# Performance work log

Measured on AMD Instinct MI355X. Metric: run time of the kernel, lower is better.

## Reference

```python
import jax, jax.numpy as jnp
import numpy as np


def setup_inputs() -> dict:
    key = jax.random.key(0)
    x = jax.random.normal(key, (16, 1, 1536, 1536), dtype=jnp.float32)
    return {"x": x, "kernel_size": 3}


def reference(x, kernel_size):
    # MaxPool2d(k, stride=k, return_indices) + MaxUnpool2d: keep only the
    # per-block argmax value in each non-overlapping k x k block, zero elsewhere.
    B, C, H, W = x.shape
    k = kernel_size
    Hk, Wk = H // k, W // k
    # [B,C,Hk,Wk,k*k] view of non-overlapping blocks
    xb = x.reshape(B, C, Hk, k, Wk, k).transpose(0, 1, 2, 4, 3, 5).reshape(B, C, Hk, Wk, k * k)
    idx = jnp.argmax(xb, axis=-1)  # first max per block, matches torch pool indices
    keep = idx[..., None] == jnp.arange(k * k)  # one-hot mask [B,C,Hk,Wk,k*k]
    out = jnp.where(keep, xb, jnp.zeros((), dtype=x.dtype))
    # scatter back to the original layout
    out = out.reshape(B, C, Hk, Wk, k, k).transpose(0, 1, 2, 4, 3, 5).reshape(B, C, H, W)
    return out
```

## Files before the change

kernel.cpp:

```cpp
#include <hip/hip_runtime.h>


#define IMG_H 1536
#define IMG_W 1536
#define N_IMG 16
#define HK    512
#define WK4   128

__global__ __launch_bounds__(256) void pool_nms_kernel(const float* __restrict__ x,
                                                       float* __restrict__ out) {
    const int tid = blockIdx.x * 256 + threadIdx.x;
    const int bw4 = tid & (WK4 - 1);
    const int t2  = tid >> 7;
    const int bh  = t2 & (HK - 1);
    const int n   = t2 >> 9;

    const size_t base = (size_t)n * (IMG_H * (size_t)IMG_W)
                      + (size_t)(bh * 3) * IMG_W
                      + (size_t)bw4 * 12;

    float row[3][12];
#pragma unroll
    for (int r = 0; r < 3; ++r) {
        const float* p = x + base + (size_t)r * IMG_W;
#pragma unroll
        for (int j = 0; j < 3; ++j) {
            float4 t = *(const float4*)(p + j * 4);
            row[r][j * 4 + 0] = t.x;
            row[r][j * 4 + 1] = t.y;
            row[r][j * 4 + 2] = t.z;
            row[r][j * 4 + 3] = t.w;
        }
    }

    float o[3][12];
#pragma unroll
    for (int s = 0; s < 4; ++s) {
        const int c0 = s * 3;
        float best = row[0][c0];
        int bi = 0;
#pragma unroll
        for (int r = 0; r < 3; ++r) {
#pragma unroll
            for (int c = 0; c < 3; ++c) {
                const float vv = row[r][c0 + c];
                if (vv > best) { best = vv; bi = r * 3 + c; }
            }
        }
#pragma unroll
        for (int r = 0; r < 3; ++r) {
#pragma unroll
            for (int c = 0; c < 3; ++c) {
                o[r][c0 + c] = ((r * 3 + c) == bi) ? row[r][c0 + c] : 0.0f;
            }
        }
    }

#pragma unroll
    for (int r = 0; r < 3; ++r) {
        float* p = out + base + (size_t)r * IMG_W;
#pragma unroll
        for (int j = 0; j < 3; ++j) {
            *(float4*)(p + j * 4) = make_float4(o[r][j * 4 + 0], o[r][j * 4 + 1],
                                                o[r][j * 4 + 2], o[r][j * 4 + 3]);
        }
    }
}

extern "C" void kernel_launch(void* const* d_in, const int* in_sizes, int n_in,
                              void* d_out, int out_size, void* d_ws, size_t ws_size,
                              hipStream_t stream) {
    const float* x = (const float*)d_in[0];
    float* out = (float*)d_out;
    const int n_threads = N_IMG * HK * WK4;
    pool_nms_kernel<<<n_threads / 256, 256, 0, stream>>>(x, out);
}
```

Before: 262.7 us.

## Stage 6-row tiles through LDS for fully coalesced global loads and stores

Each workgroup now copies a 6-row tile of the image into shared memory with contiguous float4 loads, runs the 3x3 block argmax out of LDS, writes the masked results back to LDS, then stores the tile to global memory with contiguous float4 writes. The old per-thread 48-byte strided float4 accesses were only partly coalesced, and this staging replaces them with fully coalesced streaming. The cost is 36 KB of LDS per workgroup, which limits occupancy, two barriers, and LDS bank conflicts from the 12-float stride of the per-thread access.

Result: faster. 257.5 us (-2.0%).

```diff
diff --git a/kernel.cpp b/kernel.cpp
--- a/kernel.cpp
+++ b/kernel.cpp
@@ -4,32 +4,44 @@
 #define IMG_H 1536
 #define IMG_W 1536
 #define N_IMG 16
-#define HK    512
-#define WK4   128
+#define TILE_ROWS 6
+#define TILE_F (TILE_ROWS * IMG_W)
+#define TILE_V (TILE_F / 4)
+#define V_PER_T (TILE_V / 256)
+#define TILES_PER_IMG (IMG_H / TILE_ROWS)
 
 __global__ __launch_bounds__(256) void pool_nms_kernel(const float* __restrict__ x,
                                                        float* __restrict__ out) {
-    const int tid = blockIdx.x * 256 + threadIdx.x;
-    const int bw4 = tid & (WK4 - 1);
-    const int t2  = tid >> 7;
-    const int bh  = t2 & (HK - 1);
-    const int n   = t2 >> 9;
+    __shared__ float lds[TILE_F];
 
+    const int wg = blockIdx.x;
+    const int n  = wg >> 8;
+    const int tr = wg & (TILES_PER_IMG - 1);
     const size_t base = (size_t)n * (IMG_H * (size_t)IMG_W)
-                      + (size_t)(bh * 3) * IMG_W
-                      + (size_t)bw4 * 12;
+                      + (size_t)(tr * TILE_ROWS) * IMG_W;
+    const int t = threadIdx.x;
 
+    const float4* xin = (const float4*)(x + base);
+#pragma unroll
+    for (int k = 0; k < V_PER_T; ++k) {
+        const int v = t + k * 256;
+        ((float4*)lds)[v] = xin[v];
+    }
+    __syncthreads();
+
+    const int br = t >> 7;
+    const int g  = t & 127;
     float row[3][12];
 #pragma unroll
     for (int r = 0; r < 3; ++r) {
-        const float* p = x + base + (size_t)r * IMG_W;
+        const float* p = lds + (br * 3 + r) * IMG_W + g * 12;
 #pragma unroll
         for (int j = 0; j < 3; ++j) {
-            float4 t = *(const float4*)(p + j * 4);
-            row[r][j * 4 + 0] = t.x;
-            row[r][j * 4 + 1] = t.y;
-            row[r][j * 4 + 2] = t.z;
-            row[r][j * 4 + 3] = t.w;
+            float4 v4 = *(const float4*)(p + j * 4);
+            row[r][j * 4 + 0] = v4.x;
+            row[r][j * 4 + 1] = v4.y;
+            row[r][j * 4 + 2] = v4.z;
+            row[r][j * 4 + 3] = v4.w;
         }
     }
 
@@ -58,12 +70,20 @@
 
 #pragma unroll
     for (int r = 0; r < 3; ++r) {
-        float* p = out + base + (size_t)r * IMG_W;
+        float* p = lds + (br * 3 + r) * IMG_W + g * 12;
 #pragma unroll
         for (int j = 0; j < 3; ++j) {
             *(float4*)(p + j * 4) = make_float4(o[r][j * 4 + 0], o[r][j * 4 + 1],
                                                 o[r][j * 4 + 2], o[r][j * 4 + 3]);
         }
+    }
+    __syncthreads();
+
+    float4* po = (float4*)(out + base);
+#pragma unroll
+    for (int k = 0; k < V_PER_T; ++k) {
+        const int v = t + k * 256;
+        po[v] = ((const float4*)lds)[v];
     }
 }
 
@@ -72,6 +92,6 @@
                               hipStream_t stream) {
     const float* x = (const float*)d_in[0];
     float* out = (float*)d_out;
-    const int n_threads = N_IMG * HK * WK4;
-    pool_nms_kernel<<<n_threads / 256, 256, 0, stream>>>(x, out);
+    const int n_wg = N_IMG * TILES_PER_IMG;
+    pool_nms_kernel<<<n_wg, 256, 0, stream>>>(x, out);
 }
```

## Remap threads to contiguous float4 columns with wave shuffles for block halos

Applied to the files above, without the earlier changes.

Each wavefront now covers a 256-column span of one 3-row band, and each lane loads one contiguous float4 per row, so global loads and stores are fully coalesced instead of strided 48-byte chunks per thread. Neighbouring columns of each 3x3 block are gathered with shuffle-up and shuffle-down, plus extra edge loads at span boundaries. Each lane redundantly recomputes the first-max test for every block it touches using prefix and suffix maxima. This trades extra ALU work, shuffles and halo loads for better memory coalescing.

New measurement: 258.7 us. About the same (-1.5%).

```diff
diff --git a/kernel.cpp b/kernel.cpp
--- a/kernel.cpp
+++ b/kernel.cpp
@@ -1,69 +1,100 @@
 #include <hip/hip_runtime.h>
+#include <math.h>
 
 
 #define IMG_H 1536
 #define IMG_W 1536
 #define N_IMG 16
-#define HK    512
-#define WK4   128
+#define SPANS 6
+#define BROWS 512
+
+typedef float __attribute__((ext_vector_type(4))) f32x4;
 
 __global__ __launch_bounds__(256) void pool_nms_kernel(const float* __restrict__ x,
                                                        float* __restrict__ out) {
-    const int tid = blockIdx.x * 256 + threadIdx.x;
-    const int bw4 = tid & (WK4 - 1);
-    const int t2  = tid >> 7;
-    const int bh  = t2 & (HK - 1);
-    const int n   = t2 >> 9;
+    const int lane = threadIdx.x & 63;
+    const int wid  = blockIdx.x * 4 + (threadIdx.x >> 6);
+    const int W  = wid % SPANS;
+    const int t2 = wid / SPANS;
+    const int R  = t2 & (BROWS - 1);
+    const int n  = t2 >> 9;
 
     const size_t base = (size_t)n * (IMG_H * (size_t)IMG_W)
-                      + (size_t)(bh * 3) * IMG_W
-                      + (size_t)bw4 * 12;
+                      + (size_t)(R * 3) * IMG_W;
+    const int c0 = W * 256;
+    const float* px = x + base + c0;
 
-    float row[3][12];
+    f32x4 own[3];
+#pragma unroll
+    for (int r = 0; r < 3; ++r)
+        own[r] = *(const f32x4*)(px + (size_t)r * IMG_W + lane * 4);
+
+    const int cl = (W > 0) ? -4  : 0;
+    const int cr = (W < 5) ? 256 : 252;
+    f32x4 eL[3], eR[3];
 #pragma unroll
     for (int r = 0; r < 3; ++r) {
-        const float* p = x + base + (size_t)r * IMG_W;
+        eL[r] = *(const f32x4*)(px + (size_t)r * IMG_W + cl);
+        eR[r] = *(const f32x4*)(px + (size_t)r * IMG_W + cr);
+    }
+
+    float w[3][8];
 #pragma unroll
-        for (int j = 0; j < 3; ++j) {
-            float4 t = *(const float4*)(p + j * 4);
-            row[r][j * 4 + 0] = t.x;
-            row[r][j * 4 + 1] = t.y;
-            row[r][j * 4 + 2] = t.z;
-            row[r][j * 4 + 3] = t.w;
+    for (int r = 0; r < 3; ++r) {
+        float Lz = __shfl_up(own[r].z, 1);
+        float Lw = __shfl_up(own[r].w, 1);
+        float Rx = __shfl_down(own[r].x, 1);
+        float Ry = __shfl_down(own[r].y, 1);
+        if (lane == 0)  { Lz = eL[r].z; Lw = eL[r].w; }
+        if (lane == 63) { Rx = eR[r].x; Ry = eR[r].y; }
+        w[r][0] = Lz;        w[r][1] = Lw;
+        w[r][2] = own[r].x;  w[r][3] = own[r].y;
+        w[r][4] = own[r].z;  w[r][5] = own[r].w;
+        w[r][6] = Rx;        w[r][7] = Ry;
+    }
+
+    const int lm3 = lane % 3;
+    float o_[3][4];
+#pragma unroll
+    for (int i = 0; i < 4; ++i) {
+        int m3 = lm3 + i + W;
+        m3 = (m3 >= 3) ? m3 - 3 : m3;
+        m3 = (m3 >= 3) ? m3 - 3 : m3;
+        m3 = (m3 >= 3) ? m3 - 3 : m3;
+        const bool s0 = (m3 == 0), s1 = (m3 == 1);
+
+        float b[9];
+#pragma unroll
+        for (int r = 0; r < 3; ++r)
+#pragma unroll
+            for (int j = 0; j < 3; ++j)
+                b[3 * r + j] = s0 ? w[r][i + 2 + j]
+                             : (s1 ? w[r][i + 1 + j] : w[r][i + j]);
+
+        float pm[9], sm[9];
+        pm[0] = -INFINITY;
+#pragma unroll
+        for (int k = 1; k < 9; ++k) pm[k] = fmaxf(pm[k - 1], b[k - 1]);
+        sm[8] = -INFINITY;
+#pragma unroll
+        for (int k = 7; k >= 0; --k) sm[k] = fmaxf(sm[k + 1], b[k + 1]);
+
+        bool kp[9];
+#pragma unroll
+        for (int k = 0; k < 9; ++k) kp[k] = (b[k] > pm[k]) && (b[k] >= sm[k]);
+
+#pragma unroll
+        for (int r = 0; r < 3; ++r) {
+            const bool keep = s0 ? kp[3 * r] : (s1 ? kp[3 * r + 1] : kp[3 * r + 2]);
+            o_[r][i] = keep ? w[r][i + 2] : 0.0f;
         }
     }
 
-    float o[3][12];
-#pragma unroll
-    for (int s = 0; s < 4; ++s) {
-        const int c0 = s * 3;
-        float best = row[0][c0];
-        int bi = 0;
-#pragma unroll
-        for (int r = 0; r < 3; ++r) {
-#pragma unroll
-            for (int c = 0; c < 3; ++c) {
-                const float vv = row[r][c0 + c];
-                if (vv > best) { best = vv; bi = r * 3 + c; }
-            }
-        }
-#pragma unroll
-        for (int r = 0; r < 3; ++r) {
-#pragma unroll
-            for (int c = 0; c < 3; ++c) {
-                o[r][c0 + c] = ((r * 3 + c) == bi) ? row[r][c0 + c] : 0.0f;
-            }
-        }
-    }
-
+    float* po = out + base + c0;
 #pragma unroll
     for (int r = 0; r < 3; ++r) {
-        float* p = out + base + (size_t)r * IMG_W;
-#pragma unroll
-        for (int j = 0; j < 3; ++j) {
-            *(float4*)(p + j * 4) = make_float4(o[r][j * 4 + 0], o[r][j * 4 + 1],
-                                                o[r][j * 4 + 2], o[r][j * 4 + 3]);
-        }
+        f32x4 v4 = { o_[r][0], o_[r][1], o_[r][2], o_[r][3] };
+        *(f32x4*)(po + (size_t)r * IMG_W + lane * 4) = v4;
     }
 }
 
@@ -72,6 +103,6 @@
                               hipStream_t stream) {
     const float* x = (const float*)d_in[0];
     float* out = (float*)d_out;
-    const int n_threads = N_IMG * HK * WK4;
-    pool_nms_kernel<<<n_threads / 256, 256, 0, stream>>>(x, out);
+    const int n_wg = N_IMG * BROWS * SPANS / 4;
+    pool_nms_kernel<<<n_wg, 256, 0, stream>>>(x, out);
 }
```
